# Kernel tuning notes

Hardware: AMD Instinct MI355X
Metric: run time of the kernel (lower is better)

## Reference

```python
import jax, jax.numpy as jnp
import numpy as np

EPS = 1e-8

def dice3(x, gamma, beta, alpha):
    # x: [B, L, C]; torch BatchNorm1d on transposed [B, C, L] normalizes per-channel over (B, L)
    mu = x.mean(axis=(0, 1))
    var = x.var(axis=(0, 1))  # biased, matches torch BN normalization
    xn = (x - mu) / jnp.sqrt(var + EPS) * gamma + beta
    p = jax.nn.sigmoid(xn)
    return alpha * (1.0 - p) * x + p * x

def dice2(x, gamma, beta, alpha):
    # x: [B, C]; BN per-channel over batch
    mu = x.mean(axis=0)
    var = x.var(axis=0)
    xn = (x - mu) / jnp.sqrt(var + EPS) * gamma + beta
    p = jax.nn.sigmoid(xn)
    return alpha * (1.0 - p) * x + p * x

def setup_inputs() -> dict:
    key = jax.random.key(0)
    ks = jax.random.split(key, 20)
    B, L, E = 16384, 10, 64
    N_USER = N_ITEM = 1000000
    H1, H2 = 64, 16        # LocalActivationUnit hidden_unit
    F1, F2 = 200, 80       # fc_layer hidden_units[:2]
    f32 = jnp.float32
    inp = {}
    inp['sparse_inputs'] = jax.random.randint(ks[0], (B, 2), 0, N_USER)
    inp['seqs'] = jax.random.randint(ks[1], (B, L), 0, N_ITEM)
    inp['user_table'] = jax.random.normal(ks[2], (N_USER, E), f32) * 0.02
    inp['item_table'] = jax.random.normal(ks[3], (N_ITEM, E), f32) * 0.02
    inp['his_table'] = jax.random.normal(ks[4], (N_ITEM, E), f32) * 0.02
    # LocalActivationUnit: Linear(4E->64), Dice(64,dim3), Linear(64->16), fc2 Linear(16->1)
    inp['W1'] = jax.random.normal(ks[5], (4 * E, H1), f32) * 0.05
    inp['b1'] = jnp.zeros((H1,), f32)
    inp['g1'] = jnp.ones((H1,), f32)
    inp['be1'] = jnp.zeros((H1,), f32)
    inp['a1'] = jnp.zeros((H1,), f32)
    inp['W2'] = jax.random.normal(ks[6], (H1, H2), f32) * 0.1
    inp['b2'] = jnp.zeros((H2,), f32)
    inp['Wf'] = jax.random.normal(ks[7], (H2, 1), f32) * 0.2
    inp['bf'] = jnp.zeros((1,), f32)
    # fc_layer: Linear(3E->200), Dice(200,dim2), Linear(200->80), Dice(80,dim2), Linear(80->1), sigmoid
    inp['Wa'] = jax.random.normal(ks[8], (3 * E, F1), f32) * 0.05
    inp['ba'] = jnp.zeros((F1,), f32)
    inp['ga'] = jnp.ones((F1,), f32)
    inp['bea'] = jnp.zeros((F1,), f32)
    inp['aa'] = jnp.zeros((F1,), f32)
    inp['Wb'] = jax.random.normal(ks[9], (F1, F2), f32) * 0.08
    inp['bb'] = jnp.zeros((F2,), f32)
    inp['gb'] = jnp.ones((F2,), f32)
    inp['beb'] = jnp.zeros((F2,), f32)
    inp['ab'] = jnp.zeros((F2,), f32)
    inp['Wc'] = jax.random.normal(ks[10], (F2, 1), f32) * 0.1
    inp['bc'] = jnp.zeros((1,), f32)
    return inp

def reference(sparse_inputs, seqs, user_table, item_table, his_table,
              W1, b1, g1, be1, a1, W2, b2, Wf, bf,
              Wa, ba, ga, bea, aa, Wb, bb, gb, beb, ab, Wc, bc):
    user_emb = user_table[sparse_inputs[:, 0]]          # [B, E]
    item_emb = item_table[sparse_inputs[:, 1]]          # [B, E]
    his = his_table[seqs]                               # [B, L, E]
    queries = jnp.broadcast_to(item_emb[:, None, :], his.shape)
    # concat+diff+product attention features: [B, L, 4E]
    ai = jnp.concatenate([queries, his, queries - his, queries * his], axis=-1)
    h = dice3(ai @ W1 + b1, g1, be1, a1)                # [B, L, 64]
    h = h @ W2 + b2                                     # [B, L, 16]
    score = (h @ Wf + bf)[..., 0]                       # [B, L]
    score = jnp.where(seqs == 0, 0.0, score)            # masked_fill
    pooled = jnp.einsum('bl,ble->be', score, his)       # weighted pooling
    cf = jnp.concatenate([item_emb, pooled, user_emb], axis=-1)  # [B, 3E]
    z = dice2(cf @ Wa + ba, ga, bea, aa)
    z = dice2(z @ Wb + bb, gb, beb, ab)
    out = jax.nn.sigmoid(z @ Wc + bc)                   # [B, 1]
    return out
```

## Files before the change

### kernel.cpp

```cpp
#include <hip/hip_runtime.h>
#include <hip/hip_bf16.h>

constexpr int B_   = 16384;
constexpr int L_   = 10;
constexpr int E_   = 64;
constexpr int BL_  = B_ * L_;
constexpr int H1_  = 64;
constexpr int H2_  = 16;
constexpr int CF_  = 3 * E_;
constexpr int F1_  = 200;
constexpr int F2_  = 80;

constexpr long OFF_T1    = 0;
constexpr long OFF_SCORE = 10485760;
constexpr long OFF_CF    = 10649600;
constexpr long OFF_ACC   = 13795328;
constexpr long OFF_Z1    = 0;
constexpr long OFF_Z2    = 3276800;
constexpr int  ACC_N     = 688;

typedef __bf16 bf16x8 __attribute__((ext_vector_type(8)));
typedef float  f32x4  __attribute__((ext_vector_type(4)));

__device__ __forceinline__ float sigmoidf_(float x) {
    return 1.0f / (1.0f + __expf(-x));
}

__device__ __forceinline__ unsigned short f2bf(float f) {
    unsigned u = __float_as_uint(f);
    unsigned r = (u + 0x7fffu + ((u >> 16) & 1u)) >> 16;
    return (unsigned short)r;
}
__device__ __forceinline__ unsigned pk2(float a, float b) {
    return (unsigned)f2bf(a) | ((unsigned)f2bf(b) << 16);
}

__global__ __launch_bounds__(256) void k_init(
    float* __restrict__ acc, const float* __restrict__ W1,
    unsigned short* __restrict__ W1t)
{
    int i = blockIdx.x * 256 + threadIdx.x;
    if (i < ACC_N) acc[i] = 0.0f;
    int k = i >> 6, n = i & 63;
    W1t[n * 256 + k] = f2bf(W1[i]);
}

constexpr int AROW = 132;
__global__ __launch_bounds__(256) void k_gemm1(
    const int* __restrict__ sparse, const int* __restrict__ seqs,
    const float* __restrict__ item_t, const float* __restrict__ his_t,
    const unsigned short* __restrict__ W1t, const float* __restrict__ b1,
    float* __restrict__ t1, float* __restrict__ sum1, float* __restrict__ ssq1)
{
    __shared__ unsigned As[64 * AROW];
    __shared__ float redS[4][64];
    __shared__ float redQ[4][64];

    int tid  = threadIdx.x;
    int lane = tid & 63;
    int wave = tid >> 6;
    int m    = lane & 15;
    int quad = (lane >> 4) & 3;
    int colg = 16 * wave + m;

    bf16x8 bfr[8];
    {
        const unsigned short* wp = W1t + (long)colg * 256 + quad * 8;
        #pragma unroll
        for (int kk = 0; kk < 8; kk++)
            bfr[kk] = *(const bf16x8*)(wp + kk * 32);
    }
    float bias = b1[colg];
    float ps = 0.0f, pq = 0.0f;

    for (int tile = blockIdx.x; tile < BL_ / 64; tile += gridDim.x) {
        int row0 = tile * 64;
        __syncthreads();
        #pragma unroll
        for (int t = 0; t < 8; t++) {
            int slot = t * 256 + tid;
            int p = slot & 31;
            int r = slot >> 5;
            int row = row0 + r;
            int b = (unsigned)row / 10u;
            int item = sparse[2 * b + 1];
            int hidx = seqs[row];
            float2 q2 = *(const float2*)(item_t + (long)item * 64 + 2 * p);
            float2 h2 = *(const float2*)(his_t  + (long)hidx * 64 + 2 * p);
            unsigned* a = &As[r * AROW];
            a[p]      = pk2(q2.x, q2.y);
            a[32 + p] = pk2(h2.x, h2.y);
            a[64 + p] = pk2(q2.x - h2.x, q2.y - h2.y);
            a[96 + p] = pk2(q2.x * h2.x, q2.y * h2.y);
        }
        __syncthreads();

        f32x4 acc[4] = {{0,0,0,0},{0,0,0,0},{0,0,0,0},{0,0,0,0}};
        #pragma unroll
        for (int kk = 0; kk < 8; kk++) {
            int aoff = kk * 16 + quad * 4;
            bf16x8 a0 = *(const bf16x8*)&As[( 0 + m) * AROW + aoff];
            bf16x8 a1 = *(const bf16x8*)&As[(16 + m) * AROW + aoff];
            bf16x8 a2 = *(const bf16x8*)&As[(32 + m) * AROW + aoff];
            bf16x8 a3 = *(const bf16x8*)&As[(48 + m) * AROW + aoff];
            acc[0] = __builtin_amdgcn_mfma_f32_16x16x32_bf16(a0, bfr[kk], acc[0], 0, 0, 0);
            acc[1] = __builtin_amdgcn_mfma_f32_16x16x32_bf16(a1, bfr[kk], acc[1], 0, 0, 0);
            acc[2] = __builtin_amdgcn_mfma_f32_16x16x32_bf16(a2, bfr[kk], acc[2], 0, 0, 0);
            acc[3] = __builtin_amdgcn_mfma_f32_16x16x32_bf16(a3, bfr[kk], acc[3], 0, 0, 0);
        }
        float* tb = t1 + (long)row0 * 64 + colg;
        #pragma unroll
        for (int rs = 0; rs < 4; rs++) {
            #pragma unroll
            for (int reg = 0; reg < 4; reg++) {
                float v = acc[rs][reg] + bias;
                tb[(16 * rs + quad * 4 + reg) * 64] = v;
                ps += v; pq += v * v;
            }
        }
    }

    __syncthreads();
    redS[quad][colg] = ps;
    redQ[quad][colg] = pq;
    __syncthreads();
    if (tid < 64) {
        float s = redS[0][tid] + redS[1][tid] + redS[2][tid] + redS[3][tid];
        float q = redQ[0][tid] + redQ[1][tid] + redQ[2][tid] + redQ[3][tid];
        atomicAdd(&sum1[tid], s);
        atomicAdd(&ssq1[tid], q);
    }
}

__global__ __launch_bounds__(256) void k_score(
    const float* __restrict__ t1, const int* __restrict__ seqs,
    const float* __restrict__ sum1, const float* __restrict__ ssq1,
    const float* __restrict__ g1, const float* __restrict__ be1, const float* __restrict__ a1v,
    const float* __restrict__ W2, const float* __restrict__ b2,
    const float* __restrict__ Wf, const float* __restrict__ bfv,
    float* __restrict__ score)
{
    __shared__ float As[64], Bs[64], Al[64];
    __shared__ float W2s[64 * 16];
    __shared__ float Wfs[16], b2s[16];
    int tid = threadIdx.x;
    if (tid < 64) {
        float mu = sum1[tid] * (1.0f / BL_);
        float var = ssq1[tid] * (1.0f / BL_) - mu * mu;
        float rstd = rsqrtf(var + 1e-8f);
        float A = rstd * g1[tid];
        As[tid] = A;
        Bs[tid] = be1[tid] - mu * A;
        Al[tid] = a1v[tid];
    }
    for (int i = tid; i < 64 * 16; i += 256) W2s[i] = W2[i];
    if (tid < 16) { Wfs[tid] = Wf[tid]; b2s[tid] = b2[tid]; }
    __syncthreads();

    int row = blockIdx.x * 256 + tid;
    float h[16];
    #pragma unroll
    for (int n = 0; n < 16; n++) h[n] = b2s[n];
    const float* trow = t1 + (long)row * 64;
    #pragma unroll 4
    for (int jj = 0; jj < 64; jj += 4) {
        float4 x4 = *(const float4*)(trow + jj);
        float xs[4] = {x4.x, x4.y, x4.z, x4.w};
        #pragma unroll
        for (int u = 0; u < 4; u++) {
            int j = jj + u;
            float x = xs[u];
            float xn = x * As[j] + Bs[j];
            float p = sigmoidf_(xn);
            float al = Al[j];
            float d = x * (al + p * (1.0f - al));
            #pragma unroll
            for (int n = 0; n < 16; n++) h[n] += d * W2s[j * 16 + n];
        }
    }
    float sc = bfv[0];
    #pragma unroll
    for (int n = 0; n < 16; n++) sc += h[n] * Wfs[n];
    if (seqs[row] == 0) sc = 0.0f;
    score[row] = sc;
}

__global__ __launch_bounds__(256) void k_pool(
    const int* __restrict__ sparse, const int* __restrict__ seqs,
    const float* __restrict__ user_t, const float* __restrict__ item_t,
    const float* __restrict__ his_t,
    const float* __restrict__ score, float* __restrict__ cf)
{
    int tid = threadIdx.x;
    int b = blockIdx.x * 4 + (tid >> 6);
    int e = tid & 63;
    float acc = 0.0f;
    #pragma unroll
    for (int l = 0; l < L_; l++) {
        float s = score[b * L_ + l];
        int hidx = seqs[b * L_ + l];
        acc += s * his_t[(long)hidx * 64 + e];
    }
    int uidx = sparse[2 * b];
    int iidx = sparse[2 * b + 1];
    cf[(long)b * CF_ + e]        = item_t[(long)iidx * 64 + e];
    cf[(long)b * CF_ + 64 + e]   = acc;
    cf[(long)b * CF_ + 128 + e]  = user_t[(long)uidx * 64 + e];
}

__global__ __launch_bounds__(256) void k_z1(
    const float* __restrict__ cf, const float* __restrict__ Wa, const float* __restrict__ ba,
    float* __restrict__ z1, float* __restrict__ sumA, float* __restrict__ ssqA)
{
    __shared__ float cfs[16 * CF_];
    int tid = threadIdx.x;
    int n = tid;
    float bav = (n < F1_) ? ba[n] : 0.0f;
    float ps = 0.f, pq = 0.f;

    int ntile = B_ / 16;
    for (int tile = blockIdx.x; tile < ntile; tile += gridDim.x) {
        int row0 = tile * 16;
        __syncthreads();
        for (int i = tid; i < 16 * CF_; i += 256) cfs[i] = cf[(long)row0 * CF_ + i];
        __syncthreads();
        if (n < F1_) {
            float acc[16];
            #pragma unroll
            for (int r = 0; r < 16; r++) acc[r] = 0.0f;
            for (int k = 0; k < CF_; k += 4) {
                float w0 = Wa[(long)(k + 0) * F1_ + n];
                float w1 = Wa[(long)(k + 1) * F1_ + n];
                float w2 = Wa[(long)(k + 2) * F1_ + n];
                float w3 = Wa[(long)(k + 3) * F1_ + n];
                #pragma unroll
                for (int r = 0; r < 16; r++) {
                    float4 c4 = *(const float4*)&cfs[r * CF_ + k];
                    acc[r] += c4.x * w0 + c4.y * w1 + c4.z * w2 + c4.w * w3;
                }
            }
            #pragma unroll
            for (int r = 0; r < 16; r++) {
                float v = acc[r] + bav;
                z1[(long)(row0 + r) * F1_ + n] = v;
                ps += v; pq += v * v;
            }
        }
    }
    if (n < F1_) {
        atomicAdd(&sumA[n], ps);
        atomicAdd(&ssqA[n], pq);
    }
}

__global__ __launch_bounds__(320) void k_z2(
    const float* __restrict__ z1, const float* __restrict__ Wb, const float* __restrict__ bbv,
    const float* __restrict__ sumA, const float* __restrict__ ssqA,
    const float* __restrict__ ga, const float* __restrict__ bea, const float* __restrict__ aav,
    float* __restrict__ z2, float* __restrict__ sumB, float* __restrict__ ssqB)
{
    __shared__ float zs[16 * F1_];
    __shared__ float Aa[F1_], Ba[F1_], ala[F1_];
    int tid = threadIdx.x;
    if (tid < F1_) {
        float mu = sumA[tid] * (1.0f / B_);
        float var = ssqA[tid] * (1.0f / B_) - mu * mu;
        float rstd = rsqrtf(var + 1e-8f);
        float A = rstd * ga[tid];
        Aa[tid] = A;
        Ba[tid] = bea[tid] - mu * A;
        ala[tid] = aav[tid];
    }
    int n = tid % F2_;
    int rgrp = tid / F2_;
    float bbl = bbv[n];
    float ps = 0.f, pq = 0.f;

    int ntile = B_ / 16;
    for (int tile = blockIdx.x; tile < ntile; tile += gridDim.x) {
        int row0 = tile * 16;
        __syncthreads();
        for (int i = tid; i < 16 * F1_; i += 320) {
            int k = i % F1_;
            float x = z1[(long)row0 * F1_ + i];
            float xn = x * Aa[k] + Ba[k];
            float p = sigmoidf_(xn);
            float al = ala[k];
            zs[i] = x * (al + p * (1.0f - al));
        }
        __syncthreads();
        float acc[4] = {0.f, 0.f, 0.f, 0.f};
        for (int k = 0; k < F1_; k += 4) {
            float w0 = Wb[(long)(k + 0) * F2_ + n];
            float w1 = Wb[(long)(k + 1) * F2_ + n];
            float w2 = Wb[(long)(k + 2) * F2_ + n];
            float w3 = Wb[(long)(k + 3) * F2_ + n];
            #pragma unroll
            for (int rr = 0; rr < 4; rr++) {
                float4 c4 = *(const float4*)&zs[(rgrp * 4 + rr) * F1_ + k];
                acc[rr] += c4.x * w0 + c4.y * w1 + c4.z * w2 + c4.w * w3;
            }
        }
        #pragma unroll
        for (int rr = 0; rr < 4; rr++) {
            int row = row0 + rgrp * 4 + rr;
            float v = acc[rr] + bbl;
            z2[(long)row * F2_ + n] = v;
            ps += v; pq += v * v;
        }
    }
    atomicAdd(&sumB[n], ps);
    atomicAdd(&ssqB[n], pq);
}

__global__ __launch_bounds__(256) void k_out(
    const float* __restrict__ z2,
    const float* __restrict__ sumB, const float* __restrict__ ssqB,
    const float* __restrict__ gb, const float* __restrict__ beb, const float* __restrict__ abv,
    const float* __restrict__ Wc, const float* __restrict__ bc,
    float* __restrict__ out)
{
    __shared__ float Ab[F2_], Bb[F2_], alb[F2_], Wcs[F2_];
    int tid = threadIdx.x;
    if (tid < F2_) {
        float mu = sumB[tid] * (1.0f / B_);
        float var = ssqB[tid] * (1.0f / B_) - mu * mu;
        float rstd = rsqrtf(var + 1e-8f);
        float A = rstd * gb[tid];
        Ab[tid] = A;
        Bb[tid] = beb[tid] - mu * A;
        alb[tid] = abv[tid];
        Wcs[tid] = Wc[tid];
    }
    __syncthreads();
    int row = blockIdx.x * 256 + tid;
    const float* zrow = z2 + (long)row * F2_;
    float acc = bc[0];
    #pragma unroll 4
    for (int k = 0; k < F2_; k += 4) {
        float4 x4 = *(const float4*)(zrow + k);
        float xs[4] = {x4.x, x4.y, x4.z, x4.w};
        #pragma unroll
        for (int u = 0; u < 4; u++) {
            int kk = k + u;
            float x = xs[u];
            float xn = x * Ab[kk] + Bb[kk];
            float p = sigmoidf_(xn);
            float al = alb[kk];
            float d = x * (al + p * (1.0f - al));
            acc += d * Wcs[kk];
        }
    }
    out[row] = sigmoidf_(acc);
}

extern "C" void kernel_launch(void* const* d_in, const int* in_sizes, int n_in,
                              void* d_out, int out_size, void* d_ws, size_t ws_size,
                              hipStream_t stream) {
    const int*   sparse = (const int*)  d_in[0];
    const int*   seqs   = (const int*)  d_in[1];
    const float* user_t = (const float*)d_in[2];
    const float* item_t = (const float*)d_in[3];
    const float* his_t  = (const float*)d_in[4];
    const float* W1  = (const float*)d_in[5];
    const float* b1  = (const float*)d_in[6];
    const float* g1  = (const float*)d_in[7];
    const float* be1 = (const float*)d_in[8];
    const float* a1  = (const float*)d_in[9];
    const float* W2  = (const float*)d_in[10];
    const float* b2  = (const float*)d_in[11];
    const float* Wf  = (const float*)d_in[12];
    const float* bfv = (const float*)d_in[13];
    const float* Wa  = (const float*)d_in[14];
    const float* ba  = (const float*)d_in[15];
    const float* ga  = (const float*)d_in[16];
    const float* bea = (const float*)d_in[17];
    const float* aa  = (const float*)d_in[18];
    const float* Wb  = (const float*)d_in[19];
    const float* bb  = (const float*)d_in[20];
    const float* gb  = (const float*)d_in[21];
    const float* beb = (const float*)d_in[22];
    const float* ab  = (const float*)d_in[23];
    const float* Wc  = (const float*)d_in[24];
    const float* bc  = (const float*)d_in[25];

    float* ws    = (float*)d_ws;
    float* t1    = ws + OFF_T1;
    float* score = ws + OFF_SCORE;
    float* cf    = ws + OFF_CF;
    float* acc   = ws + OFF_ACC;
    float* sum1  = acc;
    float* ssq1  = acc + 64;
    float* sumA  = acc + 128;
    float* ssqA  = acc + 328;
    float* sumB  = acc + 528;
    float* ssqB  = acc + 608;
    float* z1    = ws + OFF_Z1;
    float* z2    = ws + OFF_Z2;
    float* out   = (float*)d_out;
    unsigned short* W1t = (unsigned short*)(ws + OFF_SCORE);

    k_init<<<64, 256, 0, stream>>>(acc, W1, W1t);
    k_gemm1<<<1024, 256, 0, stream>>>(sparse, seqs, item_t, his_t, W1t, b1, t1, sum1, ssq1);
    k_score<<<BL_ / 256, 256, 0, stream>>>(t1, seqs, sum1, ssq1, g1, be1, a1, W2, b2, Wf, bfv, score);
    k_pool<<<B_ / 4, 256, 0, stream>>>(sparse, seqs, user_t, item_t, his_t, score, cf);
    k_z1<<<512, 256, 0, stream>>>(cf, Wa, ba, z1, sumA, ssqA);
    k_z2<<<512, 320, 0, stream>>>(z1, Wb, bb, sumA, ssqA, ga, bea, aa, z2, sumB, ssqB);
    k_out<<<B_ / 256, 256, 0, stream>>>(z2, sumB, ssqB, gb, beb, ab, Wc, bc, out);
}
```

Before: 743.4 us.

## Fuse attention GEMM and score via grid sync; fold W2·Wf into a vector

Merges the first attention GEMM and the score kernel into one cooperative kernel. Each block keeps its 256 rows of pre-activation results in registers, waits at a grid-wide sync for the batch-norm statistics, then applies Dice and computes scores in place. This removes the round trip of the large intermediate through global memory and one kernel launch. Because there is no nonlinearity between the second linear layer and the final projection, W2·Wf and b2·Wf+bf are precomputed into a 64-vector and a constant, so each score becomes a shuffle-reduced dot product. In exchange, all 640 blocks must be resident at once, which relies on the occupancy bound and the cooperative launch, and register pressure rises from holding 16 accumulator vectors per thread.

```diff
diff --git a/kernel.cpp b/kernel.cpp
--- a/kernel.cpp
+++ b/kernel.cpp
@@ -1,5 +1,8 @@
 #include <hip/hip_runtime.h>
 #include <hip/hip_bf16.h>
+#include <hip/hip_cooperative_groups.h>
+
+namespace cg = cooperative_groups;
 
 constexpr int B_   = 16384;
 constexpr int L_   = 10;
@@ -11,7 +14,6 @@
 constexpr int F1_  = 200;
 constexpr int F2_  = 80;
 
-constexpr long OFF_T1    = 0;
 constexpr long OFF_SCORE = 10485760;
 constexpr long OFF_CF    = 10649600;
 constexpr long OFF_ACC   = 13795328;
@@ -37,20 +39,37 @@
 
 __global__ __launch_bounds__(256) void k_init(
     float* __restrict__ acc, const float* __restrict__ W1,
-    unsigned short* __restrict__ W1t)
+    unsigned short* __restrict__ W1t,
+    const float* __restrict__ W2, const float* __restrict__ Wf,
+    const float* __restrict__ b2, const float* __restrict__ bfv,
+    float* __restrict__ wv)
 {
     int i = blockIdx.x * 256 + threadIdx.x;
     if (i < ACC_N) acc[i] = 0.0f;
+    if (i < 64) {
+        float s = 0.0f;
+        #pragma unroll
+        for (int n = 0; n < 16; n++) s += W2[i * 16 + n] * Wf[n];
+        wv[i] = s;
+    } else if (i == 64) {
+        float s = bfv[0];
+        #pragma unroll
+        for (int n = 0; n < 16; n++) s += b2[n] * Wf[n];
+        wv[64] = s;
+    }
     int k = i >> 6, n = i & 63;
     W1t[n * 256 + k] = f2bf(W1[i]);
 }
 
 constexpr int AROW = 132;
-__global__ __launch_bounds__(256) void k_gemm1(
+__global__ __launch_bounds__(256, 3) void k_gemm1(
     const int* __restrict__ sparse, const int* __restrict__ seqs,
     const float* __restrict__ item_t, const float* __restrict__ his_t,
     const unsigned short* __restrict__ W1t, const float* __restrict__ b1,
-    float* __restrict__ t1, float* __restrict__ sum1, float* __restrict__ ssq1)
+    const float* __restrict__ g1, const float* __restrict__ be1,
+    const float* __restrict__ a1v, const float* __restrict__ wv,
+    float* __restrict__ sum1, float* __restrict__ ssq1,
+    float* __restrict__ score)
 {
     __shared__ unsigned As[64 * AROW];
     __shared__ float redS[4][64];
@@ -72,9 +91,13 @@
     }
     float bias = b1[colg];
     float ps = 0.0f, pq = 0.0f;
-
-    for (int tile = blockIdx.x; tile < BL_ / 64; tile += gridDim.x) {
-        int row0 = tile * 64;
+    int row0base = blockIdx.x * 256;
+
+    f32x4 acc[4][4];
+
+    #pragma unroll
+    for (int ti = 0; ti < 4; ti++) {
+        int row0 = row0base + ti * 64;
         __syncthreads();
         #pragma unroll
         for (int t = 0; t < 8; t++) {
@@ -95,7 +118,8 @@
         }
         __syncthreads();
 
-        f32x4 acc[4] = {{0,0,0,0},{0,0,0,0},{0,0,0,0},{0,0,0,0}};
+        #pragma unroll
+        for (int rs = 0; rs < 4; rs++) acc[ti][rs] = (f32x4){0.f, 0.f, 0.f, 0.f};
         #pragma unroll
         for (int kk = 0; kk < 8; kk++) {
             int aoff = kk * 16 + quad * 4;
@@ -103,18 +127,17 @@
             bf16x8 a1 = *(const bf16x8*)&As[(16 + m) * AROW + aoff];
             bf16x8 a2 = *(const bf16x8*)&As[(32 + m) * AROW + aoff];
             bf16x8 a3 = *(const bf16x8*)&As[(48 + m) * AROW + aoff];
-            acc[0] = __builtin_amdgcn_mfma_f32_16x16x32_bf16(a0, bfr[kk], acc[0], 0, 0, 0);
-            acc[1] = __builtin_amdgcn_mfma_f32_16x16x32_bf16(a1, bfr[kk], acc[1], 0, 0, 0);
-            acc[2] = __builtin_amdgcn_mfma_f32_16x16x32_bf16(a2, bfr[kk], acc[2], 0, 0, 0);
-            acc[3] = __builtin_amdgcn_mfma_f32_16x16x32_bf16(a3, bfr[kk], acc[3], 0, 0, 0);
-        }
-        float* tb = t1 + (long)row0 * 64 + colg;
+            acc[ti][0] = __builtin_amdgcn_mfma_f32_16x16x32_bf16(a0, bfr[kk], acc[ti][0], 0, 0, 0);
+            acc[ti][1] = __builtin_amdgcn_mfma_f32_16x16x32_bf16(a1, bfr[kk], acc[ti][1], 0, 0, 0);
+            acc[ti][2] = __builtin_amdgcn_mfma_f32_16x16x32_bf16(a2, bfr[kk], acc[ti][2], 0, 0, 0);
+            acc[ti][3] = __builtin_amdgcn_mfma_f32_16x16x32_bf16(a3, bfr[kk], acc[ti][3], 0, 0, 0);
+        }
         #pragma unroll
         for (int rs = 0; rs < 4; rs++) {
             #pragma unroll
             for (int reg = 0; reg < 4; reg++) {
-                float v = acc[rs][reg] + bias;
-                tb[(16 * rs + quad * 4 + reg) * 64] = v;
+                float v = acc[ti][rs][reg] + bias;
+                acc[ti][rs][reg] = v;
                 ps += v; pq += v * v;
             }
         }
@@ -130,59 +153,45 @@
         atomicAdd(&sum1[tid], s);
         atomicAdd(&ssq1[tid], q);
     }
-}
-
-__global__ __launch_bounds__(256) void k_score(
-    const float* __restrict__ t1, const int* __restrict__ seqs,
-    const float* __restrict__ sum1, const float* __restrict__ ssq1,
-    const float* __restrict__ g1, const float* __restrict__ be1, const float* __restrict__ a1v,
-    const float* __restrict__ W2, const float* __restrict__ b2,
-    const float* __restrict__ Wf, const float* __restrict__ bfv,
-    float* __restrict__ score)
-{
-    __shared__ float As[64], Bs[64], Al[64];
-    __shared__ float W2s[64 * 16];
-    __shared__ float Wfs[16], b2s[16];
-    int tid = threadIdx.x;
-    if (tid < 64) {
-        float mu = sum1[tid] * (1.0f / BL_);
-        float var = ssq1[tid] * (1.0f / BL_) - mu * mu;
-        float rstd = rsqrtf(var + 1e-8f);
-        float A = rstd * g1[tid];
-        As[tid] = A;
-        Bs[tid] = be1[tid] - mu * A;
-        Al[tid] = a1v[tid];
-    }
-    for (int i = tid; i < 64 * 16; i += 256) W2s[i] = W2[i];
-    if (tid < 16) { Wfs[tid] = Wf[tid]; b2s[tid] = b2[tid]; }
-    __syncthreads();
-
-    int row = blockIdx.x * 256 + tid;
-    float h[16];
+    __threadfence();
+    cg::this_grid().sync();
+
+    float mu   = sum1[colg] * (1.0f / BL_);
+    float var  = ssq1[colg] * (1.0f / BL_) - mu * mu;
+    float rstd = rsqrtf(var + 1e-8f);
+    float A  = rstd * g1[colg];
+    float Bc = be1[colg] - mu * A;
+    float al = a1v[colg];
+    float wvc = wv[colg];
+    float c0  = wv[64];
+
     #pragma unroll
-    for (int n = 0; n < 16; n++) h[n] = b2s[n];
-    const float* trow = t1 + (long)row * 64;
-    #pragma unroll 4
-    for (int jj = 0; jj < 64; jj += 4) {
-        float4 x4 = *(const float4*)(trow + jj);
-        float xs[4] = {x4.x, x4.y, x4.z, x4.w};
-        #pragma unroll
-        for (int u = 0; u < 4; u++) {
-            int j = jj + u;
-            float x = xs[u];
-            float xn = x * As[j] + Bs[j];
-            float p = sigmoidf_(xn);
-            float al = Al[j];
-            float d = x * (al + p * (1.0f - al));
+    for (int ti = 0; ti < 4; ti++) {
+        int row0 = row0base + ti * 64;
+        #pragma unroll
+        for (int rs = 0; rs < 4; rs++) {
             #pragma unroll
-            for (int n = 0; n < 16; n++) h[n] += d * W2s[j * 16 + n];
-        }
-    }
-    float sc = bfv[0];
-    #pragma unroll
-    for (int n = 0; n < 16; n++) sc += h[n] * Wfs[n];
-    if (seqs[row] == 0) sc = 0.0f;
-    score[row] = sc;
+            for (int reg = 0; reg < 4; reg++) {
+                float v  = acc[ti][rs][reg];
+                float xn = v * A + Bc;
+                float p  = sigmoidf_(xn);
+                float d  = v * (al + p * (1.0f - al));
+                float c  = d * wvc;
+                c += __shfl_xor(c, 1);
+                c += __shfl_xor(c, 2);
+                c += __shfl_xor(c, 4);
+                c += __shfl_xor(c, 8);
+                if (m == 0) redS[wave][16 * rs + quad * 4 + reg] = c;
+            }
+        }
+        __syncthreads();
+        if (tid < 64) {
+            int rg = row0 + tid;
+            float sc = redS[0][tid] + redS[1][tid] + redS[2][tid] + redS[3][tid] + c0;
+            score[rg] = (seqs[rg] == 0) ? 0.0f : sc;
+        }
+        __syncthreads();
+    }
 }
 
 __global__ __launch_bounds__(256) void k_pool(
@@ -385,7 +394,6 @@
     const float* bc  = (const float*)d_in[25];
 
     float* ws    = (float*)d_ws;
-    float* t1    = ws + OFF_T1;
     float* score = ws + OFF_SCORE;
     float* cf    = ws + OFF_CF;
     float* acc   = ws + OFF_ACC;
@@ -395,14 +403,21 @@
     float* ssqA  = acc + 328;
     float* sumB  = acc + 528;
     float* ssqB  = acc + 608;
+    float* wv    = acc + 704;
     float* z1    = ws + OFF_Z1;
     float* z2    = ws + OFF_Z2;
     float* out   = (float*)d_out;
     unsigned short* W1t = (unsigned short*)(ws + OFF_SCORE);
 
-    k_init<<<64, 256, 0, stream>>>(acc, W1, W1t);
-    k_gemm1<<<1024, 256, 0, stream>>>(sparse, seqs, item_t, his_t, W1t, b1, t1, sum1, ssq1);
-    k_score<<<BL_ / 256, 256, 0, stream>>>(t1, seqs, sum1, ssq1, g1, be1, a1, W2, b2, Wf, bfv, score);
+    k_init<<<64, 256, 0, stream>>>(acc, W1, W1t, W2, Wf, b2, bfv, wv);
+    {
+        void* args[] = {
+            (void*)&sparse, (void*)&seqs, (void*)&item_t, (void*)&his_t,
+            (void*)&W1t, (void*)&b1, (void*)&g1, (void*)&be1, (void*)&a1,
+            (void*)&wv, (void*)&sum1, (void*)&ssq1, (void*)&score
+        };
+        hipLaunchCooperativeKernel(k_gemm1, dim3(640), dim3(256), args, 0, stream);
+    }
     k_pool<<<B_ / 4, 256, 0, stream>>>(sparse, seqs, user_t, item_t, his_t, score, cf);
     k_z1<<<512, 256, 0, stream>>>(cf, Wa, ba, z1, sumA, ssqA);
     k_z2<<<512, 320, 0, stream>>>(z1, Wb, bb, sumA, ssqA, ga, bea, aa, z2, sumB, ssqB);
```

New measurement: 858.7 us. 1.16x slower.

## Cache gathered history rows, swizzle gemm1 LDS, one tile per block, retile z1

Applied to the files above, without the earlier changes.

gemm1 now processes one 64-row tile per block with occupancy launch bounds and an XOR-swizzled LDS layout in place of padding. It also writes the gathered history embeddings to a contiguous workspace buffer, so the pooling kernel streams rows instead of doing random gathers from the large table. The z1 kernel is retiled to 32 rows per block with float4 weight loads, four columns and eight rows per thread, and a block-level reduction before the atomics. The trade-off is extra workspace writes, a larger grid that issues more atomics, and a workspace offset that has to avoid overlapping other buffers.

```diff
diff --git a/kernel.cpp b/kernel.cpp
--- a/kernel.cpp
+++ b/kernel.cpp
@@ -15,6 +15,7 @@
 constexpr long OFF_SCORE = 10485760;
 constexpr long OFF_CF    = 10649600;
 constexpr long OFF_ACC   = 13795328;
+constexpr long OFF_HISC  = 13796352;
 constexpr long OFF_Z1    = 0;
 constexpr long OFF_Z2    = 3276800;
 constexpr int  ACC_N     = 688;
@@ -45,16 +46,14 @@
     W1t[n * 256 + k] = f2bf(W1[i]);
 }
 
-constexpr int AROW = 132;
-__global__ __launch_bounds__(256) void k_gemm1(
+__global__ __launch_bounds__(256, 5) void k_gemm1(
     const int* __restrict__ sparse, const int* __restrict__ seqs,
     const float* __restrict__ item_t, const float* __restrict__ his_t,
     const unsigned short* __restrict__ W1t, const float* __restrict__ b1,
-    float* __restrict__ t1, float* __restrict__ sum1, float* __restrict__ ssq1)
-{
-    __shared__ unsigned As[64 * AROW];
-    __shared__ float redS[4][64];
-    __shared__ float redQ[4][64];
+    float* __restrict__ t1, float* __restrict__ hisc,
+    float* __restrict__ sum1, float* __restrict__ ssq1)
+{
+    __shared__ unsigned As[64 * 128];
 
     int tid  = threadIdx.x;
     int lane = tid & 63;
@@ -71,62 +70,65 @@
             bfr[kk] = *(const bf16x8*)(wp + kk * 32);
     }
     float bias = b1[colg];
+    int row0 = blockIdx.x * 64;
+
+    #pragma unroll 4
+    for (int t = 0; t < 8; t++) {
+        int slot = t * 256 + tid;
+        int p = slot & 31;
+        int r = slot >> 5;
+        int row = row0 + r;
+        int b = (unsigned)row / 10u;
+        int item = sparse[2 * b + 1];
+        int hidx = seqs[row];
+        float2 q2 = *(const float2*)(item_t + (long)item * 64 + 2 * p);
+        float2 h2 = *(const float2*)(his_t  + (long)hidx * 64 + 2 * p);
+        *(float2*)(hisc + (long)row * 64 + 2 * p) = h2;
+        unsigned sw = (unsigned)(r & 7) << 2;
+        unsigned* a = &As[r * 128];
+        unsigned ps_ = p ^ sw;
+        a[ps_]      = pk2(q2.x, q2.y);
+        a[32 + ps_] = pk2(h2.x, h2.y);
+        a[64 + ps_] = pk2(q2.x - h2.x, q2.y - h2.y);
+        a[96 + ps_] = pk2(q2.x * h2.x, q2.y * h2.y);
+    }
+    __syncthreads();
+
+    f32x4 acc[4] = {{0,0,0,0},{0,0,0,0},{0,0,0,0},{0,0,0,0}};
+    unsigned swm = (unsigned)(m & 7) << 2;
+    #pragma unroll
+    for (int kk = 0; kk < 8; kk++) {
+        unsigned aoff = (unsigned)(kk * 16 + quad * 4);
+        unsigned c = (aoff & ~31u) + ((aoff & 31u) ^ swm);
+        bf16x8 a0 = *(const bf16x8*)&As[( 0 + m) * 128 + c];
+        bf16x8 a1 = *(const bf16x8*)&As[(16 + m) * 128 + c];
+        bf16x8 a2 = *(const bf16x8*)&As[(32 + m) * 128 + c];
+        bf16x8 a3 = *(const bf16x8*)&As[(48 + m) * 128 + c];
+        acc[0] = __builtin_amdgcn_mfma_f32_16x16x32_bf16(a0, bfr[kk], acc[0], 0, 0, 0);
+        acc[1] = __builtin_amdgcn_mfma_f32_16x16x32_bf16(a1, bfr[kk], acc[1], 0, 0, 0);
+        acc[2] = __builtin_amdgcn_mfma_f32_16x16x32_bf16(a2, bfr[kk], acc[2], 0, 0, 0);
+        acc[3] = __builtin_amdgcn_mfma_f32_16x16x32_bf16(a3, bfr[kk], acc[3], 0, 0, 0);
+    }
     float ps = 0.0f, pq = 0.0f;
-
-    for (int tile = blockIdx.x; tile < BL_ / 64; tile += gridDim.x) {
-        int row0 = tile * 64;
-        __syncthreads();
-        #pragma unroll
-        for (int t = 0; t < 8; t++) {
-            int slot = t * 256 + tid;
-            int p = slot & 31;
-            int r = slot >> 5;
-            int row = row0 + r;
-            int b = (unsigned)row / 10u;
-            int item = sparse[2 * b + 1];
-            int hidx = seqs[row];
-            float2 q2 = *(const float2*)(item_t + (long)item * 64 + 2 * p);
-            float2 h2 = *(const float2*)(his_t  + (long)hidx * 64 + 2 * p);
-            unsigned* a = &As[r * AROW];
-            a[p]      = pk2(q2.x, q2.y);
-            a[32 + p] = pk2(h2.x, h2.y);
-            a[64 + p] = pk2(q2.x - h2.x, q2.y - h2.y);
-            a[96 + p] = pk2(q2.x * h2.x, q2.y * h2.y);
-        }
-        __syncthreads();
-
-        f32x4 acc[4] = {{0,0,0,0},{0,0,0,0},{0,0,0,0},{0,0,0,0}};
-        #pragma unroll
-        for (int kk = 0; kk < 8; kk++) {
-            int aoff = kk * 16 + quad * 4;
-            bf16x8 a0 = *(const bf16x8*)&As[( 0 + m) * AROW + aoff];
-            bf16x8 a1 = *(const bf16x8*)&As[(16 + m) * AROW + aoff];
-            bf16x8 a2 = *(const bf16x8*)&As[(32 + m) * AROW + aoff];
-            bf16x8 a3 = *(const bf16x8*)&As[(48 + m) * AROW + aoff];
-            acc[0] = __builtin_amdgcn_mfma_f32_16x16x32_bf16(a0, bfr[kk], acc[0], 0, 0, 0);
-            acc[1] = __builtin_amdgcn_mfma_f32_16x16x32_bf16(a1, bfr[kk], acc[1], 0, 0, 0);
-            acc[2] = __builtin_amdgcn_mfma_f32_16x16x32_bf16(a2, bfr[kk], acc[2], 0, 0, 0);
-            acc[3] = __builtin_amdgcn_mfma_f32_16x16x32_bf16(a3, bfr[kk], acc[3], 0, 0, 0);
-        }
-        float* tb = t1 + (long)row0 * 64 + colg;
-        #pragma unroll
-        for (int rs = 0; rs < 4; rs++) {
-            #pragma unroll
-            for (int reg = 0; reg < 4; reg++) {
-                float v = acc[rs][reg] + bias;
-                tb[(16 * rs + quad * 4 + reg) * 64] = v;
-                ps += v; pq += v * v;
-            }
-        }
-    }
-
-    __syncthreads();
-    redS[quad][colg] = ps;
-    redQ[quad][colg] = pq;
+    float* tb = t1 + (long)row0 * 64 + colg;
+    #pragma unroll
+    for (int rs = 0; rs < 4; rs++) {
+        #pragma unroll
+        for (int reg = 0; reg < 4; reg++) {
+            float v = acc[rs][reg] + bias;
+            tb[(16 * rs + quad * 4 + reg) * 64] = v;
+            ps += v; pq += v * v;
+        }
+    }
+
+    __syncthreads();
+    float* red = (float*)As;
+    red[quad * 64 + colg]       = ps;
+    red[256 + quad * 64 + colg] = pq;
     __syncthreads();
     if (tid < 64) {
-        float s = redS[0][tid] + redS[1][tid] + redS[2][tid] + redS[3][tid];
-        float q = redQ[0][tid] + redQ[1][tid] + redQ[2][tid] + redQ[3][tid];
+        float s = red[tid] + red[64 + tid] + red[128 + tid] + red[192 + tid];
+        float q = red[256 + tid] + red[320 + tid] + red[384 + tid] + red[448 + tid];
         atomicAdd(&sum1[tid], s);
         atomicAdd(&ssq1[tid], q);
     }
@@ -186,9 +188,9 @@
 }
 
 __global__ __launch_bounds__(256) void k_pool(
-    const int* __restrict__ sparse, const int* __restrict__ seqs,
+    const int* __restrict__ sparse,
     const float* __restrict__ user_t, const float* __restrict__ item_t,
-    const float* __restrict__ his_t,
+    const float* __restrict__ hisc,
     const float* __restrict__ score, float* __restrict__ cf)
 {
     int tid = threadIdx.x;
@@ -198,8 +200,7 @@
     #pragma unroll
     for (int l = 0; l < L_; l++) {
         float s = score[b * L_ + l];
-        int hidx = seqs[b * L_ + l];
-        acc += s * his_t[(long)hidx * 64 + e];
+        acc += s * hisc[(long)(b * L_ + l) * 64 + e];
     }
     int uidx = sparse[2 * b];
     int iidx = sparse[2 * b + 1];
@@ -212,44 +213,60 @@
     const float* __restrict__ cf, const float* __restrict__ Wa, const float* __restrict__ ba,
     float* __restrict__ z1, float* __restrict__ sumA, float* __restrict__ ssqA)
 {
-    __shared__ float cfs[16 * CF_];
+    __shared__ float cfs[32 * CF_];
     int tid = threadIdx.x;
-    int n = tid;
-    float bav = (n < F1_) ? ba[n] : 0.0f;
-    float ps = 0.f, pq = 0.f;
-
-    int ntile = B_ / 16;
-    for (int tile = blockIdx.x; tile < ntile; tile += gridDim.x) {
-        int row0 = tile * 16;
-        __syncthreads();
-        for (int i = tid; i < 16 * CF_; i += 256) cfs[i] = cf[(long)row0 * CF_ + i];
-        __syncthreads();
-        if (n < F1_) {
-            float acc[16];
+    int row0 = blockIdx.x * 32;
+
+    for (int i = tid; i < 32 * CF_ / 4; i += 256)
+        ((float4*)cfs)[i] = ((const float4*)(cf + (long)row0 * CF_))[i];
+    __syncthreads();
+
+    float4 accv[8];
+    int cp = tid % 50, rh = tid / 50;
+    float psj[4] = {0,0,0,0}, pqj[4] = {0,0,0,0};
+    if (tid < 200) {
+        #pragma unroll
+        for (int r = 0; r < 8; r++) accv[r] = make_float4(0.f, 0.f, 0.f, 0.f);
+        for (int kk = 0; kk < CF_ / 4; kk++) {
+            float4 w0 = *(const float4*)(Wa + (long)(4 * kk + 0) * F1_ + 4 * cp);
+            float4 w1 = *(const float4*)(Wa + (long)(4 * kk + 1) * F1_ + 4 * cp);
+            float4 w2 = *(const float4*)(Wa + (long)(4 * kk + 2) * F1_ + 4 * cp);
+            float4 w3 = *(const float4*)(Wa + (long)(4 * kk + 3) * F1_ + 4 * cp);
             #pragma unroll
-            for (int r = 0; r < 16; r++) acc[r] = 0.0f;
-            for (int k = 0; k < CF_; k += 4) {
-                float w0 = Wa[(long)(k + 0) * F1_ + n];
-                float w1 = Wa[(long)(k + 1) * F1_ + n];
-                float w2 = Wa[(long)(k + 2) * F1_ + n];
-                float w3 = Wa[(long)(k + 3) * F1_ + n];
-                #pragma unroll
-                for (int r = 0; r < 16; r++) {
-                    float4 c4 = *(const float4*)&cfs[r * CF_ + k];
-                    acc[r] += c4.x * w0 + c4.y * w1 + c4.z * w2 + c4.w * w3;
-                }
+            for (int r = 0; r < 8; r++) {
+                float4 c = *(const float4*)&cfs[(8 * rh + r) * CF_ + 4 * kk];
+                accv[r].x += c.x * w0.x + c.y * w1.x + c.z * w2.x + c.w * w3.x;
+                accv[r].y += c.x * w0.y + c.y * w1.y + c.z * w2.y + c.w * w3.y;
+                accv[r].z += c.x * w0.z + c.y * w1.z + c.z * w2.z + c.w * w3.z;
+                accv[r].w += c.x * w0.w + c.y * w1.w + c.z * w2.w + c.w * w3.w;
             }
-            #pragma unroll
-            for (int r = 0; r < 16; r++) {
-                float v = acc[r] + bav;
-                z1[(long)(row0 + r) * F1_ + n] = v;
-                ps += v; pq += v * v;
-            }
-        }
-    }
-    if (n < F1_) {
-        atomicAdd(&sumA[n], ps);
-        atomicAdd(&ssqA[n], pq);
+        }
+        float4 bav = *(const float4*)(ba + 4 * cp);
+        #pragma unroll
+        for (int r = 0; r < 8; r++) {
+            float4 v = make_float4(accv[r].x + bav.x, accv[r].y + bav.y,
+                                   accv[r].z + bav.z, accv[r].w + bav.w);
+            *(float4*)(z1 + (long)(row0 + 8 * rh + r) * F1_ + 4 * cp) = v;
+            psj[0] += v.x; pqj[0] += v.x * v.x;
+            psj[1] += v.y; pqj[1] += v.y * v.y;
+            psj[2] += v.z; pqj[2] += v.z * v.z;
+            psj[3] += v.w; pqj[3] += v.w * v.w;
+        }
+    }
+    __syncthreads();
+    if (tid < 200) {
+        #pragma unroll
+        for (int j = 0; j < 4; j++) {
+            cfs[rh * 200 + 4 * cp + j]       = psj[j];
+            cfs[800 + rh * 200 + 4 * cp + j] = pqj[j];
+        }
+    }
+    __syncthreads();
+    if (tid < F1_) {
+        float s = cfs[tid] + cfs[200 + tid] + cfs[400 + tid] + cfs[600 + tid];
+        float q = cfs[800 + tid] + cfs[1000 + tid] + cfs[1200 + tid] + cfs[1400 + tid];
+        atomicAdd(&sumA[tid], s);
+        atomicAdd(&ssqA[tid], q);
     }
 }
 
@@ -389,6 +406,7 @@
     float* score = ws + OFF_SCORE;
     float* cf    = ws + OFF_CF;
     float* acc   = ws + OFF_ACC;
+    float* hisc  = ws + OFF_HISC;
     float* sum1  = acc;
     float* ssq1  = acc + 64;
     float* sumA  = acc + 128;
@@ -401,10 +419,10 @@
     unsigned short* W1t = (unsigned short*)(ws + OFF_SCORE);
 
     k_init<<<64, 256, 0, stream>>>(acc, W1, W1t);
-    k_gemm1<<<1024, 256, 0, stream>>>(sparse, seqs, item_t, his_t, W1t, b1, t1, sum1, ssq1);
+    k_gemm1<<<BL_ / 64, 256, 0, stream>>>(sparse, seqs, item_t, his_t, W1t, b1, t1, hisc, sum1, ssq1);
     k_score<<<BL_ / 256, 256, 0, stream>>>(t1, seqs, sum1, ssq1, g1, be1, a1, W2, b2, Wf, bfv, score);
-    k_pool<<<B_ / 4, 256, 0, stream>>>(sparse, seqs, user_t, item_t, his_t, score, cf);
-    k_z1<<<512, 256, 0, stream>>>(cf, Wa, ba, z1, sumA, ssqA);
+    k_pool<<<B_ / 4, 256, 0, stream>>>(sparse, user_t, item_t, hisc, score, cf);
+    k_z1<<<B_ / 32, 256, 0, stream>>>(cf, Wa, ba, z1, sumA, ssqA);
     k_z2<<<512, 320, 0, stream>>>(z1, Wb, bb, sumA, ssqA, ga, bea, aa, z2, sumB, ssqB);
     k_out<<<B_ / 256, 256, 0, stream>>>(z2, sumB, ssqB, gb, beb, ab, Wc, bc, out);
 }
```

Result: no change. 758.1 us (+2.0%).
